# Kernel optimization log

Hardware: AMD Instinct MI355X
Metric: run time of the kernel (lower is better)

The kernel has to match this reference:

```python
import jax, jax.numpy as jnp
import numpy as np

B, E, D, H, A = 65536, 16, 256, 64, 18  # batch, n_subpolicies, emb_dim, hidden, n_actions


def setup_inputs() -> dict:
    key = jax.random.key(0)
    ks = jax.random.split(key, 16)
    s = lambda k, sh: jax.random.normal(k, sh, dtype=jnp.float32) * 0.05
    return dict(
        obs=s(ks[0], (B, D)),
        h=s(ks[1], (B, D)),
        c=s(ks[2], (B, D)),
        idxs=jax.random.randint(ks[3], (B,), 0, E, dtype=jnp.int32),
        # Observer: LSTMCell(D, D) params (torch layout: [4D, D] with i,f,g,o gate order)
        W_ih=s(ks[4], (4 * D, D)), W_hh=s(ks[5], (4 * D, D)),
        b_ih=s(ks[6], (4 * D,)), b_hh=s(ks[7], (4 * D,)),
        # Stacked SubPolicy actor params: Linear(D,64)-Tanh-Linear(64,A)
        Wa1=s(ks[8], (E, D, H)), ba1=s(ks[9], (E, H)),
        Wa2=s(ks[10], (E, H, A)), ba2=s(ks[11], (E, A)),
        # Stacked SubPolicy critic params: Linear(D,64)-Tanh-Linear(64,1)
        Wc1=s(ks[12], (E, D, H)), bc1=s(ks[13], (E, H)),
        Wc2=s(ks[14], (E, H, 1)), bc2=s(ks[15], (E, 1)),
    )


def reference(obs, h, c, idxs, W_ih, W_hh, b_ih, b_hh,
              Wa1, ba1, Wa2, ba2, Wc1, bc1, Wc2, bc2):
    # ---- Observer: single LSTMCell step ----
    gates = obs @ W_ih.T + b_ih + h @ W_hh.T + b_hh          # [B, 4D]
    gi, gf, gg, go = jnp.split(gates, 4, axis=1)
    i = jax.nn.sigmoid(gi); f = jax.nn.sigmoid(gf); o = jax.nn.sigmoid(go)
    c_new = f * c + i * jnp.tanh(gg)                          # [B, D]
    h_new = o * jnp.tanh(c_new)                               # [B, D]

    # ---- Expert dispatch: evaluate all tiny subpolicy MLPs, select per sample ----
    # (mathematically identical to the per-sample routing loop in forward_sub)
    ha = jnp.tanh(jnp.einsum('bd,edh->beh', h_new, Wa1) + ba1)        # [B, E, H]
    logits_all = jnp.einsum('beh,eha->bea', ha, Wa2) + ba2            # [B, E, A]
    hc = jnp.tanh(jnp.einsum('bd,edh->beh', h_new, Wc1) + bc1)        # [B, E, H]
    vals_all = (jnp.einsum('beh,eho->beo', hc, Wc2) + bc2)[..., 0]    # [B, E]

    b = jnp.arange(h_new.shape[0])
    logits = logits_all[b, idxs]                                       # [B, A]
    values = vals_all[b, idxs]                                         # [B]
    return (h_new, c_new, logits, values)
```

## Files before the change

### kernel.cpp

```cpp
#include <hip/hip_runtime.h>
#include <hip/hip_bf16.h>
#include <math.h>

#define NB 65536
#define ND 256
#define NE 16
#define NH 64
#define NA 18

typedef __bf16 bf16;
typedef __bf16 bf16x4 __attribute__((ext_vector_type(4)));
typedef __bf16 bf16x8 __attribute__((ext_vector_type(8)));
typedef float  f32x4  __attribute__((ext_vector_type(4)));

#define OFF_WCAT 0u
#define OFF_BCAT 1048576u
#define OFF_PW1  1052672u
#define OFF_B1   2101248u
#define OFF_CUR  2109440u
#define OFF_PERM 2109504u

__device__ __forceinline__ float rcp_(float x) { return __builtin_amdgcn_rcpf(x); }
__device__ __forceinline__ float sigm_(float x) { return rcp_(1.f + __expf(-x)); }
__device__ __forceinline__ float tanh_(float x) {
    float cl = fminf(fmaxf(x, -15.f), 15.f);
    float e = __expf(2.f * cl);
    return (e - 1.f) * rcp_(e + 1.f);
}

__device__ __forceinline__ void gl2lds16(const void* g, void* l) {
    __builtin_amdgcn_global_load_lds(
        (const __attribute__((address_space(1))) unsigned int*)g,
        (__attribute__((address_space(3))) unsigned int*)l, 16, 0, 0);
}

__global__ void k_prep1(const float* __restrict__ W_ih, const float* __restrict__ W_hh,
                        const float* __restrict__ b_ih, const float* __restrict__ b_hh,
                        char* __restrict__ ws) {
    int t = blockIdx.x * 256 + threadIdx.x;
    int kstep = t >> 13;
    int cb    = (t >> 11) & 3;
    int idx   = t & 2047;
    int kf = idx >> 10, g = (idx >> 8) & 3, lk = (idx >> 6) & 3, u = idx & 63;
    int col = g * 256 + cb * 64 + (u ^ lk);
    int k0  = kstep * 64 + (kf * 4 + lk) * 8;
    const float* src = (k0 < 256) ? (W_ih + (size_t)col * 256 + k0)
                                  : (W_hh + (size_t)col * 256 + (k0 - 256));
    float4 v0 = *(const float4*)(src);
    float4 v1 = *(const float4*)(src + 4);
    bf16x8 o;
    o[0] = (bf16)v0.x; o[1] = (bf16)v0.y; o[2] = (bf16)v0.z; o[3] = (bf16)v0.w;
    o[4] = (bf16)v1.x; o[5] = (bf16)v1.y; o[6] = (bf16)v1.z; o[7] = (bf16)v1.w;
    *(bf16x8*)((bf16*)(ws + OFF_WCAT) + (size_t)t * 8) = o;
    if (t < 1024) ((float*)(ws + OFF_BCAT))[t] = b_ih[t] + b_hh[t];
    if (t < 16)   ((int*)(ws + OFF_CUR))[t] = t * 65536;
}

__global__ void k_prep2(const float* __restrict__ Wa1, const float* __restrict__ Wc1,
                        const float* __restrict__ ba1, const float* __restrict__ bc1,
                        char* __restrict__ ws) {
    int t = blockIdx.x * 256 + threadIdx.x;
    bf16* PW1 = (bf16*)(ws + OFF_PW1);
    int col = t & 127, kc = (t >> 7) & 31, e = t >> 12;
    bf16x8 o;
#pragma unroll
    for (int j = 0; j < 8; ++j) {
        int k = kc * 8 + j;
        float v = (col < 64) ? Wa1[((size_t)e * 256 + k) * 64 + col]
                             : Wc1[((size_t)e * 256 + k) * 64 + (col - 64)];
        o[j] = (bf16)v;
    }
    *(bf16x8*)(PW1 + (((size_t)e * 32 + kc) * 128 + col) * 8) = o;
    if (t < 2048) {
        int e2 = t >> 7, c = t & 127;
        ((float*)(ws + OFF_B1))[t] = (c < 64) ? ba1[e2 * 64 + c] : bc1[e2 * 64 + (c - 64)];
    }
}

__global__ void k_scatter(const int* __restrict__ idxs, char* __restrict__ ws) {
    __shared__ int lh[16], lbase[16];
    int t = threadIdx.x;
    int i = blockIdx.x * 256 + t;
    if (t < 16) lh[t] = 0;
    __syncthreads();
    int e = idxs[i];
    int r = atomicAdd(&lh[e], 1);
    __syncthreads();
    int* cur = (int*)(ws + OFF_CUR);
    if (t < 16) lbase[t] = atomicAdd(&cur[t], lh[t]);
    __syncthreads();
    ((int*)(ws + OFF_PERM))[lbase[e] + r] = i;
}

__global__ __launch_bounds__(256, 3) void k_lstm(
    const float* __restrict__ obs, const float* __restrict__ hin,
    const float* __restrict__ cin, const float* __restrict__ bcat,
    const char* __restrict__ wcat,
    float* __restrict__ hout, float* __restrict__ cout) {
    __shared__ alignas(16) char Abuf[2][8192];
    __shared__ alignas(16) char Bbuf[32768];
    const int tid  = threadIdx.x;
    const int w = tid >> 6, lane = tid & 63;
    const int lr = lane & 15, lk = lane >> 4;
    const int bid = blockIdx.x;
    const int xcd = bid & 7, rest = bid >> 3;
    const int cb = rest & 3;
    const int rb = ((rest >> 2) << 3) | xcd;
    const int row0 = rb * 64;
    const int colc = cb * 64 + w * 16 + lr;
    const int srw = tid >> 3, sj = tid & 7;

    const char* WcatBlk = wcat + (size_t)cb * 32768;
    const float* baseO0 = obs + (size_t)(row0 + srw) * 256 + sj * 8;
    const float* baseH0 = hin + (size_t)(row0 + srw) * 256 + sj * 8;

    int offE[4], offO[4];
#pragma unroll
    for (int m = 0; m < 4; ++m) {
        int R = m * 16 + lr;
        offE[m] = lk * 1024 + ((R ^ lk) * 16);
        offO[m] = (lk + 4) * 1024 + ((R ^ (lk + 4)) * 16);
    }
    const int bBase = lk * 1024 + (((w * 16 + lr) ^ lk) * 16);

    f32x4 acc[4][4];
#pragma unroll
    for (int m = 0; m < 4; ++m)
#pragma unroll
        for (int g = 0; g < 4; ++g)
#pragma unroll
            for (int r = 0; r < 4; ++r) acc[m][g][r] = 0.f;

#define STAGE_B(ks)                                                          \
    {                                                                        \
        const char* srcB_ = WcatBlk + (size_t)(ks) * 131072;                 \
        _Pragma("unroll")                                                    \
        for (int i_ = 0; i_ < 8; ++i_) {                                     \
            int so_ = (w * 8 + i_) * 1024;                                   \
            gl2lds16(srcB_ + so_ + lane * 16, &Bbuf[so_]);                   \
        }                                                                    \
    }
#define LOAD_A(ks)                                                           \
    {                                                                        \
        const float* s0_ = ((ks) < 4) ? (baseO0 + (ks) * 64)                 \
                                      : (baseH0 + ((ks) - 4) * 64);          \
        pf0 = *(const float4*)(s0_);                                         \
        pf1 = *(const float4*)(s0_ + 4);                                     \
        pf2 = *(const float4*)(s0_ + 32 * 256);                              \
        pf3 = *(const float4*)(s0_ + 32 * 256 + 4);                          \
    }
#define WRITE_A(bi)                                                          \
    {                                                                        \
        bf16x8 oa_, ob_;                                                     \
        oa_[0] = (bf16)pf0.x; oa_[1] = (bf16)pf0.y; oa_[2] = (bf16)pf0.z;    \
        oa_[3] = (bf16)pf0.w; oa_[4] = (bf16)pf1.x; oa_[5] = (bf16)pf1.y;    \
        oa_[6] = (bf16)pf1.z; oa_[7] = (bf16)pf1.w;                          \
        ob_[0] = (bf16)pf2.x; ob_[1] = (bf16)pf2.y; ob_[2] = (bf16)pf2.z;    \
        ob_[3] = (bf16)pf2.w; ob_[4] = (bf16)pf3.x; ob_[5] = (bf16)pf3.y;    \
        ob_[6] = (bf16)pf3.z; ob_[7] = (bf16)pf3.w;                          \
        *(bf16x8*)(&Abuf[bi][sj * 1024 + ((srw ^ sj) * 16)]) = oa_;          \
        *(bf16x8*)(&Abuf[bi][sj * 1024 + (((srw + 32) ^ sj) * 16)]) = ob_;   \
    }
#define MFMA_HALF(cur, offA, q0, q1, q2, q3)                                 \
    {                                                                        \
        const char* Ab_ = Abuf[cur];                                         \
        bf16x8 a0 = *(const bf16x8*)(Ab_ + offA[0]);                         \
        bf16x8 a1 = *(const bf16x8*)(Ab_ + offA[1]);                         \
        bf16x8 a2 = *(const bf16x8*)(Ab_ + offA[2]);                         \
        bf16x8 a3 = *(const bf16x8*)(Ab_ + offA[3]);                         \
        acc[0][0] = __builtin_amdgcn_mfma_f32_16x16x32_bf16(a0, q0, acc[0][0], 0, 0, 0); \
        acc[1][0] = __builtin_amdgcn_mfma_f32_16x16x32_bf16(a1, q0, acc[1][0], 0, 0, 0); \
        acc[2][0] = __builtin_amdgcn_mfma_f32_16x16x32_bf16(a2, q0, acc[2][0], 0, 0, 0); \
        acc[3][0] = __builtin_amdgcn_mfma_f32_16x16x32_bf16(a3, q0, acc[3][0], 0, 0, 0); \
        acc[0][1] = __builtin_amdgcn_mfma_f32_16x16x32_bf16(a0, q1, acc[0][1], 0, 0, 0); \
        acc[1][1] = __builtin_amdgcn_mfma_f32_16x16x32_bf16(a1, q1, acc[1][1], 0, 0, 0); \
        acc[2][1] = __builtin_amdgcn_mfma_f32_16x16x32_bf16(a2, q1, acc[2][1], 0, 0, 0); \
        acc[3][1] = __builtin_amdgcn_mfma_f32_16x16x32_bf16(a3, q1, acc[3][1], 0, 0, 0); \
        acc[0][2] = __builtin_amdgcn_mfma_f32_16x16x32_bf16(a0, q2, acc[0][2], 0, 0, 0); \
        acc[1][2] = __builtin_amdgcn_mfma_f32_16x16x32_bf16(a1, q2, acc[1][2], 0, 0, 0); \
        acc[2][2] = __builtin_amdgcn_mfma_f32_16x16x32_bf16(a2, q2, acc[2][2], 0, 0, 0); \
        acc[3][2] = __builtin_amdgcn_mfma_f32_16x16x32_bf16(a3, q2, acc[3][2], 0, 0, 0); \
        acc[0][3] = __builtin_amdgcn_mfma_f32_16x16x32_bf16(a0, q3, acc[0][3], 0, 0, 0); \
        acc[1][3] = __builtin_amdgcn_mfma_f32_16x16x32_bf16(a1, q3, acc[1][3], 0, 0, 0); \
        acc[2][3] = __builtin_amdgcn_mfma_f32_16x16x32_bf16(a2, q3, acc[2][3], 0, 0, 0); \
        acc[3][3] = __builtin_amdgcn_mfma_f32_16x16x32_bf16(a3, q3, acc[3][3], 0, 0, 0); \
    }

    float4 pf0, pf1, pf2, pf3;
    float cpre[16];

    LOAD_A(0);
    STAGE_B(0);
    WRITE_A(0);
    LOAD_A(1);
    __syncthreads();

#pragma unroll
    for (int t = 0; t < 8; ++t) {
        const int cur = t & 1;
        const char* Bb0 = Bbuf + bBase;
        bf16x8 br0 = *(const bf16x8*)(Bb0);
        bf16x8 br1 = *(const bf16x8*)(Bb0 + 4096);
        bf16x8 br2 = *(const bf16x8*)(Bb0 + 8192);
        bf16x8 br3 = *(const bf16x8*)(Bb0 + 12288);
        bf16x8 br4 = *(const bf16x8*)(Bb0 + 16384);
        bf16x8 br5 = *(const bf16x8*)(Bb0 + 20480);
        bf16x8 br6 = *(const bf16x8*)(Bb0 + 24576);
        bf16x8 br7 = *(const bf16x8*)(Bb0 + 28672);
        __syncthreads();
        if (t == 6) {
#pragma unroll
            for (int m = 0; m < 4; ++m)
#pragma unroll
                for (int r = 0; r < 4; ++r)
                    cpre[m * 4 + r] = cin[(size_t)(row0 + m * 16 + lk * 4 + r) * 256 + colc];
        }
        if (t < 7) {
            STAGE_B(t + 1);
            WRITE_A(cur ^ 1);
        }
        if (t < 6) LOAD_A(t + 2);
        MFMA_HALF(cur, offE, br0, br1, br2, br3);
        MFMA_HALF(cur, offO, br4, br5, br6, br7);
        if (t < 7) __syncthreads();
    }
#undef STAGE_B
#undef LOAD_A
#undef WRITE_A
#undef MFMA_HALF

    float bi = bcat[colc], bf_ = bcat[256 + colc], bg = bcat[512 + colc], bo = bcat[768 + colc];
#pragma unroll
    for (int m = 0; m < 4; ++m) {
#pragma unroll
        for (int r = 0; r < 4; ++r) {
            int row = row0 + m * 16 + lk * 4 + r;
            float gi = acc[m][0][r] + bi;
            float gf = acc[m][1][r] + bf_;
            float gg = acc[m][2][r] + bg;
            float go = acc[m][3][r] + bo;
            float iv = sigm_(gi), fv = sigm_(gf), gv = tanh_(gg), ov = sigm_(go);
            float cn = fv * cpre[m * 4 + r] + iv * gv;
            float hn = ov * tanh_(cn);
            cout[(size_t)row * 256 + colc] = cn;
            hout[(size_t)row * 256 + colc] = hn;
        }
    }
}

__global__ __launch_bounds__(256) void k_expert(
    const float* __restrict__ Wa2, const float* __restrict__ ba2,
    const float* __restrict__ Wc2, const float* __restrict__ bc2,
    char* __restrict__ ws, const float* __restrict__ hsrc,
    float* __restrict__ lout, float* __restrict__ vout) {
    const int e = blockIdx.y;
    const int* cur = (const int*)(ws + OFF_CUR);
    int cnt = cur[e] - e * 65536;
    int r0 = blockIdx.x * 64;
    if (r0 >= cnt) return;
    int nr = min(64, cnt - r0);
    const int* permE = (const int*)(ws + OFF_PERM) + (size_t)e * 65536 + r0;

    __shared__ int rows_s[64];
    __shared__ alignas(16) char smem[128 * 66 * 4];
    bf16*  Alds = (bf16*)smem;
    float* haF  = (float*)smem;

    int t = threadIdx.x;
    if (t < 64) rows_s[t] = permE[(t < nr) ? t : 0];
    __syncthreads();

    {
        int rowi = t >> 2, q = t & 3;
        const float* hp = hsrc + (size_t)rows_s[rowi] * 256;
#pragma unroll
        for (int s = 0; s < 8; ++s) {
            int kc = s * 4 + q;
            float4 v0 = *(const float4*)(hp + kc * 8);
            float4 v1 = *(const float4*)(hp + kc * 8 + 4);
            bf16x8 o;
            o[0] = (bf16)v0.x; o[1] = (bf16)v0.y; o[2] = (bf16)v0.z; o[3] = (bf16)v0.w;
            o[4] = (bf16)v1.x; o[5] = (bf16)v1.y; o[6] = (bf16)v1.z; o[7] = (bf16)v1.w;
            *(bf16x8*)(Alds + ((size_t)kc * 64 + rowi) * 8) = o;
        }
    }
    __syncthreads();

    const bf16* PW1 = (const bf16*)(ws + OFF_PW1) + (size_t)e * 32 * 128 * 8;
    const float* b1 = (const float*)(ws + OFF_B1) + e * 128;
    int wave = t >> 6, lane = t & 63, lr = lane & 15, lk = lane >> 4;

    f32x4 acc[4][2];
#pragma unroll
    for (int m = 0; m < 4; ++m)
#pragma unroll
        for (int n = 0; n < 2; ++n)
#pragma unroll
            for (int r = 0; r < 4; ++r) acc[m][n][r] = 0.f;

#pragma unroll
    for (int kf = 0; kf < 8; ++kf) {
        bf16x8 a[4], bb[2];
#pragma unroll
        for (int m = 0; m < 4; ++m)
            a[m] = *(const bf16x8*)(Alds + (((kf * 4 + lk) * 64) + (m * 16 + lr)) * 8);
#pragma unroll
        for (int n = 0; n < 2; ++n) {
            int colh = wave * 32 + n * 16 + lr;
            int kc = kf * 4 + lk;
            bb[n] = *(const bf16x8*)(PW1 + ((size_t)kc * 128 + colh) * 8);
        }
#pragma unroll
        for (int m = 0; m < 4; ++m)
#pragma unroll
            for (int n = 0; n < 2; ++n)
                acc[m][n] = __builtin_amdgcn_mfma_f32_16x16x32_bf16(a[m], bb[n], acc[m][n], 0, 0, 0);
    }
    __syncthreads();

#pragma unroll
    for (int m = 0; m < 4; ++m)
#pragma unroll
        for (int n = 0; n < 2; ++n) {
            int colh = wave * 32 + n * 16 + lr;
            float bbv = b1[colh];
#pragma unroll
            for (int r = 0; r < 4; ++r) {
                int row = m * 16 + lk * 4 + r;
                haF[colh * 66 + row] = tanh_(acc[m][n][r] + bbv);
            }
        }
    __syncthreads();

    int row = t & 63;
    int grow = rows_s[row];
    bool valid = row < nr;
#pragma unroll
    for (int p = 0; p < 5; ++p) {
        int aI = p * 4 + (t >> 6);
        if (aI < NA) {
            float s = ba2[e * NA + aI];
            for (int hh = 0; hh < 64; ++hh)
                s += haF[hh * 66 + row] * Wa2[((size_t)e * 64 + hh) * NA + aI];
            if (valid) lout[(size_t)grow * NA + aI] = s;
        }
    }
    if (t < 64) {
        float s = bc2[e];
        for (int hh = 0; hh < 64; ++hh)
            s += haF[(64 + hh) * 66 + row] * Wc2[e * 64 + hh];
        if (valid) vout[grow] = s;
    }
}

extern "C" void kernel_launch(void* const* d_in, const int* in_sizes, int n_in,
                              void* d_out, int out_size, void* d_ws, size_t ws_size,
                              hipStream_t stream) {
    const float* obs  = (const float*)d_in[0];
    const float* h    = (const float*)d_in[1];
    const float* c    = (const float*)d_in[2];
    const int*   idxs = (const int*)d_in[3];
    const float* W_ih = (const float*)d_in[4];
    const float* W_hh = (const float*)d_in[5];
    const float* b_ih = (const float*)d_in[6];
    const float* b_hh = (const float*)d_in[7];
    const float* Wa1  = (const float*)d_in[8];
    const float* ba1  = (const float*)d_in[9];
    const float* Wa2  = (const float*)d_in[10];
    const float* ba2  = (const float*)d_in[11];
    const float* Wc1  = (const float*)d_in[12];
    const float* bc1  = (const float*)d_in[13];
    const float* Wc2  = (const float*)d_in[14];
    const float* bc2  = (const float*)d_in[15];

    float* out  = (float*)d_out;
    float* hout = out;
    float* cout = out + (size_t)NB * ND;
    float* lout = out + (size_t)2 * NB * ND;
    float* vout = lout + (size_t)NB * NA;
    char* ws = (char*)d_ws;

    k_prep1<<<dim3(256), dim3(256), 0, stream>>>(W_ih, W_hh, b_ih, b_hh, ws);
    k_prep2<<<dim3(256), dim3(256), 0, stream>>>(Wa1, Wc1, ba1, bc1, ws);
    k_scatter<<<dim3(256), dim3(256), 0, stream>>>(idxs, ws);
    k_lstm<<<dim3(4096), dim3(256), 0, stream>>>(
        obs, h, c, (const float*)(ws + OFF_BCAT), (const char*)(ws + OFF_WCAT), hout, cout);
    k_expert<<<dim3(1024, 16), dim3(256), 0, stream>>>(
        Wa2, ba2, Wc2, bc2, ws, hout, lout, vout);
}
```

Baseline: 199.9 us.

## Double LSTM GEMM row tile to 128 and stage epilogue through LDS

Each LSTM block now covers 128 rows instead of 64, so every staged weight tile is reused across twice as many rows. This halves the grid and doubles the accumulator registers, and occupancy drops from 3 to 2 blocks per unit. The cell-state input is now read with coalesced float4 loads and staged in LDS, and the h/c outputs are written back as coalesced float4 rows, replacing the strided scalar global accesses. The cost is more LDS per block, extra barriers in the epilogue and higher register pressure.

```diff
diff --git a/kernel.cpp b/kernel.cpp
--- a/kernel.cpp
+++ b/kernel.cpp
@@ -92,40 +92,40 @@
     ((int*)(ws + OFF_PERM))[lbase[e] + r] = i;
 }
 
-__global__ __launch_bounds__(256, 3) void k_lstm(
+__global__ __launch_bounds__(256, 2) void k_lstm(
     const float* __restrict__ obs, const float* __restrict__ hin,
     const float* __restrict__ cin, const float* __restrict__ bcat,
     const char* __restrict__ wcat,
     float* __restrict__ hout, float* __restrict__ cout) {
-    __shared__ alignas(16) char Abuf[2][8192];
+    __shared__ alignas(16) char Abuf[2][16384];
     __shared__ alignas(16) char Bbuf[32768];
     const int tid  = threadIdx.x;
     const int w = tid >> 6, lane = tid & 63;
     const int lr = lane & 15, lk = lane >> 4;
     const int bid = blockIdx.x;
-    const int xcd = bid & 7, rest = bid >> 3;
-    const int cb = rest & 3;
-    const int rb = ((rest >> 2) << 3) | xcd;
-    const int row0 = rb * 64;
+    const int xcd = bid & 7;
+    const int cb  = (bid >> 3) & 3;
+    const int rb  = ((bid >> 5) << 3) | xcd;
+    const int row0 = rb * 128;
     const int colc = cb * 64 + w * 16 + lr;
-    const int srw = tid >> 3, sj = tid & 7;
+    const int srw = tid >> 1, sf = tid & 1;
 
     const char* WcatBlk = wcat + (size_t)cb * 32768;
-    const float* baseO0 = obs + (size_t)(row0 + srw) * 256 + sj * 8;
-    const float* baseH0 = hin + (size_t)(row0 + srw) * 256 + sj * 8;
-
-    int offE[4], offO[4];
-#pragma unroll
-    for (int m = 0; m < 4; ++m) {
+    const float* baseO0 = obs + (size_t)(row0 + srw) * 256 + sf * 32;
+    const float* baseH0 = hin + (size_t)(row0 + srw) * 256 + sf * 32;
+
+    int offE[8], offO[8];
+#pragma unroll
+    for (int m = 0; m < 8; ++m) {
         int R = m * 16 + lr;
-        offE[m] = lk * 1024 + ((R ^ lk) * 16);
-        offO[m] = (lk + 4) * 1024 + ((R ^ (lk + 4)) * 16);
+        offE[m] = lk * 2048 + ((R ^ lk) * 16);
+        offO[m] = (lk + 4) * 2048 + ((R ^ (lk + 4)) * 16);
     }
     const int bBase = lk * 1024 + (((w * 16 + lr) ^ lk) * 16);
 
-    f32x4 acc[4][4];
-#pragma unroll
-    for (int m = 0; m < 4; ++m)
+    f32x4 acc[8][4];
+#pragma unroll
+    for (int m = 0; m < 8; ++m)
 #pragma unroll
         for (int g = 0; g < 4; ++g)
 #pragma unroll
@@ -144,50 +144,67 @@
     {                                                                        \
         const float* s0_ = ((ks) < 4) ? (baseO0 + (ks) * 64)                 \
                                       : (baseH0 + ((ks) - 4) * 64);          \
-        pf0 = *(const float4*)(s0_);                                         \
-        pf1 = *(const float4*)(s0_ + 4);                                     \
-        pf2 = *(const float4*)(s0_ + 32 * 256);                              \
-        pf3 = *(const float4*)(s0_ + 32 * 256 + 4);                          \
+        pf0 = *(const float4*)(s0_);      pf1 = *(const float4*)(s0_ + 4);   \
+        pf2 = *(const float4*)(s0_ + 8);  pf3 = *(const float4*)(s0_ + 12);  \
+        pf4 = *(const float4*)(s0_ + 16); pf5 = *(const float4*)(s0_ + 20);  \
+        pf6 = *(const float4*)(s0_ + 24); pf7 = *(const float4*)(s0_ + 28);  \
+    }
+#define CVW(bi, q, va, vb)                                                   \
+    {                                                                        \
+        int kc_ = sf * 4 + (q);                                              \
+        bf16x8 o_;                                                           \
+        o_[0] = (bf16)va.x; o_[1] = (bf16)va.y; o_[2] = (bf16)va.z;          \
+        o_[3] = (bf16)va.w; o_[4] = (bf16)vb.x; o_[5] = (bf16)vb.y;          \
+        o_[6] = (bf16)vb.z; o_[7] = (bf16)vb.w;                              \
+        *(bf16x8*)(&Abuf[bi][kc_ * 2048 + ((srw ^ kc_) * 16)]) = o_;         \
     }
 #define WRITE_A(bi)                                                          \
-    {                                                                        \
-        bf16x8 oa_, ob_;                                                     \
-        oa_[0] = (bf16)pf0.x; oa_[1] = (bf16)pf0.y; oa_[2] = (bf16)pf0.z;    \
-        oa_[3] = (bf16)pf0.w; oa_[4] = (bf16)pf1.x; oa_[5] = (bf16)pf1.y;    \
-        oa_[6] = (bf16)pf1.z; oa_[7] = (bf16)pf1.w;                          \
-        ob_[0] = (bf16)pf2.x; ob_[1] = (bf16)pf2.y; ob_[2] = (bf16)pf2.z;    \
-        ob_[3] = (bf16)pf2.w; ob_[4] = (bf16)pf3.x; ob_[5] = (bf16)pf3.y;    \
-        ob_[6] = (bf16)pf3.z; ob_[7] = (bf16)pf3.w;                          \
-        *(bf16x8*)(&Abuf[bi][sj * 1024 + ((srw ^ sj) * 16)]) = oa_;          \
-        *(bf16x8*)(&Abuf[bi][sj * 1024 + (((srw + 32) ^ sj) * 16)]) = ob_;   \
-    }
+    { CVW(bi, 0, pf0, pf1); CVW(bi, 1, pf2, pf3);                            \
+      CVW(bi, 2, pf4, pf5); CVW(bi, 3, pf6, pf7); }
 #define MFMA_HALF(cur, offA, q0, q1, q2, q3)                                 \
     {                                                                        \
         const char* Ab_ = Abuf[cur];                                         \
-        bf16x8 a0 = *(const bf16x8*)(Ab_ + offA[0]);                         \
-        bf16x8 a1 = *(const bf16x8*)(Ab_ + offA[1]);                         \
-        bf16x8 a2 = *(const bf16x8*)(Ab_ + offA[2]);                         \
-        bf16x8 a3 = *(const bf16x8*)(Ab_ + offA[3]);                         \
-        acc[0][0] = __builtin_amdgcn_mfma_f32_16x16x32_bf16(a0, q0, acc[0][0], 0, 0, 0); \
-        acc[1][0] = __builtin_amdgcn_mfma_f32_16x16x32_bf16(a1, q0, acc[1][0], 0, 0, 0); \
-        acc[2][0] = __builtin_amdgcn_mfma_f32_16x16x32_bf16(a2, q0, acc[2][0], 0, 0, 0); \
-        acc[3][0] = __builtin_amdgcn_mfma_f32_16x16x32_bf16(a3, q0, acc[3][0], 0, 0, 0); \
-        acc[0][1] = __builtin_amdgcn_mfma_f32_16x16x32_bf16(a0, q1, acc[0][1], 0, 0, 0); \
-        acc[1][1] = __builtin_amdgcn_mfma_f32_16x16x32_bf16(a1, q1, acc[1][1], 0, 0, 0); \
-        acc[2][1] = __builtin_amdgcn_mfma_f32_16x16x32_bf16(a2, q1, acc[2][1], 0, 0, 0); \
-        acc[3][1] = __builtin_amdgcn_mfma_f32_16x16x32_bf16(a3, q1, acc[3][1], 0, 0, 0); \
-        acc[0][2] = __builtin_amdgcn_mfma_f32_16x16x32_bf16(a0, q2, acc[0][2], 0, 0, 0); \
-        acc[1][2] = __builtin_amdgcn_mfma_f32_16x16x32_bf16(a1, q2, acc[1][2], 0, 0, 0); \
-        acc[2][2] = __builtin_amdgcn_mfma_f32_16x16x32_bf16(a2, q2, acc[2][2], 0, 0, 0); \
-        acc[3][2] = __builtin_amdgcn_mfma_f32_16x16x32_bf16(a3, q2, acc[3][2], 0, 0, 0); \
-        acc[0][3] = __builtin_amdgcn_mfma_f32_16x16x32_bf16(a0, q3, acc[0][3], 0, 0, 0); \
-        acc[1][3] = __builtin_amdgcn_mfma_f32_16x16x32_bf16(a1, q3, acc[1][3], 0, 0, 0); \
-        acc[2][3] = __builtin_amdgcn_mfma_f32_16x16x32_bf16(a2, q3, acc[2][3], 0, 0, 0); \
-        acc[3][3] = __builtin_amdgcn_mfma_f32_16x16x32_bf16(a3, q3, acc[3][3], 0, 0, 0); \
-    }
-
-    float4 pf0, pf1, pf2, pf3;
-    float cpre[16];
+        _Pragma("unroll")                                                    \
+        for (int m = 0; m < 8; ++m) {                                        \
+            bf16x8 a_ = *(const bf16x8*)(Ab_ + offA[m]);                     \
+            acc[m][0] = __builtin_amdgcn_mfma_f32_16x16x32_bf16(a_, q0, acc[m][0], 0, 0, 0); \
+            acc[m][1] = __builtin_amdgcn_mfma_f32_16x16x32_bf16(a_, q1, acc[m][1], 0, 0, 0); \
+            acc[m][2] = __builtin_amdgcn_mfma_f32_16x16x32_bf16(a_, q2, acc[m][2], 0, 0, 0); \
+            acc[m][3] = __builtin_amdgcn_mfma_f32_16x16x32_bf16(a_, q3, acc[m][3], 0, 0, 0); \
+        }                                                                    \
+    }
+#define PIPE_STEP(T)                                                         \
+    {                                                                        \
+        const int CUR = (T) & 1;                                             \
+        const char* Bb0 = Bbuf + bBase;                                      \
+        bf16x8 br0 = *(const bf16x8*)(Bb0);                                  \
+        bf16x8 br1 = *(const bf16x8*)(Bb0 + 4096);                           \
+        bf16x8 br2 = *(const bf16x8*)(Bb0 + 8192);                           \
+        bf16x8 br3 = *(const bf16x8*)(Bb0 + 12288);                          \
+        bf16x8 br4 = *(const bf16x8*)(Bb0 + 16384);                          \
+        bf16x8 br5 = *(const bf16x8*)(Bb0 + 20480);                          \
+        bf16x8 br6 = *(const bf16x8*)(Bb0 + 24576);                          \
+        bf16x8 br7 = *(const bf16x8*)(Bb0 + 28672);                          \
+        __syncthreads();                            \
+        if ((T) < 7) {                                                       \
+            STAGE_B((T) + 1);                       \
+            WRITE_A(CUR ^ 1);                       \
+        }                                                                    \
+        if ((T) < 6) LOAD_A((T) + 2);                                        \
+        if ((T) == 6) {                           \
+            const float* cs_ = cin + (size_t)(row0 + srw) * 256 + cb * 64 + sf * 32; \
+            ci0 = *(const float4*)(cs_);      ci1 = *(const float4*)(cs_ + 4);  \
+            ci2 = *(const float4*)(cs_ + 8);  ci3 = *(const float4*)(cs_ + 12); \
+            ci4 = *(const float4*)(cs_ + 16); ci5 = *(const float4*)(cs_ + 20); \
+            ci6 = *(const float4*)(cs_ + 24); ci7 = *(const float4*)(cs_ + 28); \
+        }                                                                    \
+        MFMA_HALF(CUR, offE, br0, br1, br2, br3);                            \
+        MFMA_HALF(CUR, offO, br4, br5, br6, br7);                            \
+        __syncthreads();                          \
+    }
+
+    float4 pf0, pf1, pf2, pf3, pf4, pf5, pf6, pf7;
+    float4 ci0, ci1, ci2, ci3, ci4, ci5, ci6, ci7;
 
     LOAD_A(0);
     STAGE_B(0);
@@ -195,57 +212,68 @@
     LOAD_A(1);
     __syncthreads();
 
-#pragma unroll
-    for (int t = 0; t < 8; ++t) {
-        const int cur = t & 1;
-        const char* Bb0 = Bbuf + bBase;
-        bf16x8 br0 = *(const bf16x8*)(Bb0);
-        bf16x8 br1 = *(const bf16x8*)(Bb0 + 4096);
-        bf16x8 br2 = *(const bf16x8*)(Bb0 + 8192);
-        bf16x8 br3 = *(const bf16x8*)(Bb0 + 12288);
-        bf16x8 br4 = *(const bf16x8*)(Bb0 + 16384);
-        bf16x8 br5 = *(const bf16x8*)(Bb0 + 20480);
-        bf16x8 br6 = *(const bf16x8*)(Bb0 + 24576);
-        bf16x8 br7 = *(const bf16x8*)(Bb0 + 28672);
-        __syncthreads();
-        if (t == 6) {
-#pragma unroll
-            for (int m = 0; m < 4; ++m)
-#pragma unroll
-                for (int r = 0; r < 4; ++r)
-                    cpre[m * 4 + r] = cin[(size_t)(row0 + m * 16 + lk * 4 + r) * 256 + colc];
-        }
-        if (t < 7) {
-            STAGE_B(t + 1);
-            WRITE_A(cur ^ 1);
-        }
-        if (t < 6) LOAD_A(t + 2);
-        MFMA_HALF(cur, offE, br0, br1, br2, br3);
-        MFMA_HALF(cur, offO, br4, br5, br6, br7);
-        if (t < 7) __syncthreads();
-    }
+    PIPE_STEP(0); PIPE_STEP(1); PIPE_STEP(2); PIPE_STEP(3);
+    PIPE_STEP(4); PIPE_STEP(5); PIPE_STEP(6); PIPE_STEP(7);
+
 #undef STAGE_B
 #undef LOAD_A
+#undef CVW
 #undef WRITE_A
 #undef MFMA_HALF
-
-    float bi = bcat[colc], bf_ = bcat[256 + colc], bg = bcat[512 + colc], bo = bcat[768 + colc];
-#pragma unroll
-    for (int m = 0; m < 4; ++m) {
-#pragma unroll
-        for (int r = 0; r < 4; ++r) {
-            int row = row0 + m * 16 + lk * 4 + r;
-            float gi = acc[m][0][r] + bi;
-            float gf = acc[m][1][r] + bf_;
-            float gg = acc[m][2][r] + bg;
-            float go = acc[m][3][r] + bo;
-            float iv = sigm_(gi), fv = sigm_(gf), gv = tanh_(gg), ov = sigm_(go);
-            float cn = fv * cpre[m * 4 + r] + iv * gv;
-            float hn = ov * tanh_(cn);
-            cout[(size_t)row * 256 + colc] = cn;
-            hout[(size_t)row * 256 + colc] = hn;
-        }
-    }
+#undef PIPE_STEP
+
+#define EPI(row, s) ((row) * 256 + ((((s) ^ ((row) & 15))) * 16))
+    char* CNbuf = (char*)Abuf;
+    *(float4*)(&Bbuf[EPI(srw, sf * 8 + 0)]) = ci0;
+    *(float4*)(&Bbuf[EPI(srw, sf * 8 + 1)]) = ci1;
+    *(float4*)(&Bbuf[EPI(srw, sf * 8 + 2)]) = ci2;
+    *(float4*)(&Bbuf[EPI(srw, sf * 8 + 3)]) = ci3;
+    *(float4*)(&Bbuf[EPI(srw, sf * 8 + 4)]) = ci4;
+    *(float4*)(&Bbuf[EPI(srw, sf * 8 + 5)]) = ci5;
+    *(float4*)(&Bbuf[EPI(srw, sf * 8 + 6)]) = ci6;
+    *(float4*)(&Bbuf[EPI(srw, sf * 8 + 7)]) = ci7;
+    __syncthreads();
+
+    {
+        float bi = bcat[colc], bf_ = bcat[256 + colc], bg = bcat[512 + colc], bo = bcat[768 + colc];
+        const int cwi = w * 16 + lr;
+        const int s_  = cwi >> 2, word_ = (cwi & 3) * 4;
+#pragma unroll
+        for (int m = 0; m < 8; ++m) {
+#pragma unroll
+            for (int r = 0; r < 4; ++r) {
+                int rl = m * 16 + lk * 4 + r;
+                int ea = EPI(rl, s_) + word_;
+                float co = *(const float*)(&Bbuf[ea]);
+                float gi = acc[m][0][r] + bi;
+                float gf = acc[m][1][r] + bf_;
+                float gg = acc[m][2][r] + bg;
+                float go = acc[m][3][r] + bo;
+                float iv = sigm_(gi), fv = sigm_(gf), gv = tanh_(gg), ov = sigm_(go);
+                float cn = fv * co + iv * gv;
+                float hn = ov * tanh_(cn);
+                *(float*)(&CNbuf[ea]) = cn;
+                *(float*)(&Bbuf[ea])  = hn;
+            }
+        }
+    }
+    __syncthreads();
+
+    {
+        float* cO = cout + (size_t)(row0 + srw) * 256 + cb * 64 + sf * 32;
+        float* hO = hout + (size_t)(row0 + srw) * 256 + cb * 64 + sf * 32;
+#pragma unroll
+        for (int j = 0; j < 8; ++j) {
+            float4 vc = *(const float4*)(&CNbuf[EPI(srw, sf * 8 + j)]);
+            *(float4*)(cO + j * 4) = vc;
+        }
+#pragma unroll
+        for (int j = 0; j < 8; ++j) {
+            float4 vh = *(const float4*)(&Bbuf[EPI(srw, sf * 8 + j)]);
+            *(float4*)(hO + j * 4) = vh;
+        }
+    }
+#undef EPI
 }
 
 __global__ __launch_bounds__(256) void k_expert(
@@ -383,7 +411,7 @@
     k_prep1<<<dim3(256), dim3(256), 0, stream>>>(W_ih, W_hh, b_ih, b_hh, ws);
     k_prep2<<<dim3(256), dim3(256), 0, stream>>>(Wa1, Wc1, ba1, bc1, ws);
     k_scatter<<<dim3(256), dim3(256), 0, stream>>>(idxs, ws);
-    k_lstm<<<dim3(4096), dim3(256), 0, stream>>>(
+    k_lstm<<<dim3(2048), dim3(256), 0, stream>>>(
         obs, h, c, (const float*)(ws + OFF_BCAT), (const char*)(ws + OFF_WCAT), hout, cout);
     k_expert<<<dim3(1024, 16), dim3(256), 0, stream>>>(
         Wa2, ba2, Wc2, bc2, ws, hout, lout, vout);
```

After: 228.0 us. 14.1% more time.
